# Optimization experiments

Hardware: AMD Instinct MI355X
Metric: run time of the kernel (lower is better)

The kernel has to match this reference:

```python
import jax, jax.numpy as jnp
import numpy as np

N_NODES = 100000
N_EDGES = 1600000
IN_DIM = 10
HID = 64
OUT_DIM = 2


def _gcn_norm(edge_index, num_nodes):
    # PyG gcn_norm with add_self_loops=False, edge_weight=1
    src, dst = edge_index[0], edge_index[1]
    deg = jnp.zeros((num_nodes,), jnp.float32).at[dst].add(1.0)
    dinv = jnp.where(deg > 0, jax.lax.rsqrt(deg), 0.0)
    return dinv[src] * dinv[dst]  # [E]


def _arma_conv(x, edge_index, norm, W, V, b):
    # ARMAConv, num_stacks=1, num_layers=1 (PyG defaults):
    # out = A_norm @ (x @ W_init) + x @ V_root + b   (no internal act at T=1)
    src, dst = edge_index[0], edge_index[1]
    h = x @ W                                   # [N, F_out]
    msg = norm[:, None] * h[src]                # [E, F_out] gather
    agg = jax.ops.segment_sum(msg, dst, num_segments=x.shape[0])  # scatter-add
    return agg + x @ V + b


def setup_inputs() -> dict:
    key = jax.random.key(0)
    ks = jax.random.split(key, 9)
    x = jax.random.uniform(ks[0], (N_NODES, IN_DIM), dtype=jnp.float32)
    edge_index = jax.random.randint(ks[1], (2, N_EDGES), 0, N_NODES, dtype=jnp.int64)
    s = 0.1
    W1 = jax.random.normal(ks[2], (IN_DIM, HID), jnp.float32) * s
    V1 = jax.random.normal(ks[3], (IN_DIM, HID), jnp.float32) * s
    b1 = jnp.zeros((HID,), jnp.float32)
    W2 = jax.random.normal(ks[4], (HID, HID), jnp.float32) * s
    V2 = jax.random.normal(ks[5], (HID, HID), jnp.float32) * s
    b2 = jnp.zeros((HID,), jnp.float32)
    W3 = jax.random.normal(ks[6], (HID, OUT_DIM), jnp.float32) * s
    V3 = jax.random.normal(ks[7], (HID, OUT_DIM), jnp.float32) * s
    b3 = jnp.zeros((OUT_DIM,), jnp.float32)
    return {"x": x, "edge_index": edge_index,
            "W1": W1, "V1": V1, "b1": b1,
            "W2": W2, "V2": V2, "b2": b2,
            "W3": W3, "V3": V3, "b3": b3}


def reference(x, edge_index, W1, V1, b1, W2, V2, b2, W3, V3, b3):
    norm = _gcn_norm(edge_index, x.shape[0])
    h = jax.nn.relu(_arma_conv(x, edge_index, norm, W1, V1, b1))
    # dropout is identity at eval time
    h = jax.nn.relu(_arma_conv(h, edge_index, norm, W2, V2, b2))
    h = _arma_conv(h, edge_index, norm, W3, V3, b3)
    return jax.nn.log_softmax(h, axis=1)
```

## Files before the change

### kernel.cpp

```cpp
#include <hip/hip_runtime.h>
#include <hip/hip_fp16.h>
#include <math.h>

#define NN 100000
#define NE 1600000
#define HID 64
#define BN 128
#define NBUCK 782
#define FBCAP 2304
#define NSB 49
#define SBCAP 34816
#define CHUNK1 4096
#define NBLK1 391
#define CSTRIDE 32

__device__ __forceinline__ __half2 shfl_xor_h2(__half2 v, int m) {
    unsigned int u = *(unsigned int*)&v;
    u = __shfl_xor(u, m);
    return *(__half2*)&u;
}
__device__ __forceinline__ unsigned int h2bits(__half2 v) {
    return *(unsigned int*)&v;
}


__global__ void k_zero_i(int* __restrict__ p, int n) {
    int i = blockIdx.x * blockDim.x + threadIdx.x;
    if (i < n) p[i] = 0;
}


__global__ __launch_bounds__(256) void k_binA1(const int* __restrict__ src,
                                               const int* __restrict__ dst,
                                               int* __restrict__ bcur1,
                                               unsigned int* __restrict__ sbdata) {
    __shared__ unsigned int par[CHUNK1];
    __shared__ unsigned short rnk[CHUNK1];
    __shared__ unsigned char bkt[CHUNK1];
    __shared__ int hist[NSB];
    __shared__ int base[NSB];
    int tid = threadIdx.x;
    int e0 = blockIdx.x * CHUNK1;
    int m = NE - e0; if (m > CHUNK1) m = CHUNK1;
    if (tid < NSB) hist[tid] = 0;
    __syncthreads();
    for (int i = tid; i < m; i += 256) {
        int s = src[e0 + i], d = dst[e0 + i];
        int b = d >> 11;
        par[i] = (unsigned int)s | ((unsigned int)(d & 2047) << 17);
        bkt[i] = (unsigned char)b;
        rnk[i] = (unsigned short)atomicAdd(&hist[b], 1);
    }
    __syncthreads();
    if (tid < NSB) {
        int h = hist[tid];
        base[tid] = h ? atomicAdd(&bcur1[tid * CSTRIDE], h) : 0;
    }
    __syncthreads();
    for (int i = tid; i < m; i += 256) {
        int b = bkt[i];
        int pos = base[b] + rnk[i];
        if (pos < SBCAP) sbdata[(size_t)b * SBCAP + pos] = par[i];
    }
}

__global__ __launch_bounds__(256) void k_binA2(const int* __restrict__ bcur1,
                                               const unsigned int* __restrict__ sbdata,
                                               int* __restrict__ bcur2,
                                               unsigned int* __restrict__ fbdata) {
    __shared__ unsigned int par[4352];
    __shared__ unsigned short rnk[4352];
    __shared__ unsigned char bkt[4352];
    __shared__ int hist[16];
    __shared__ int base[16];
    int tid = threadIdx.x;
    int sb = blockIdx.x >> 3, sl = blockIdx.x & 7;
    int m = bcur1[sb * CSTRIDE]; if (m > SBCAP) m = SBCAP;
    int L = (m + 7) >> 3;
    int lo = sl * L;
    int cnt = m - lo; if (cnt > L) cnt = L; if (cnt < 0) cnt = 0;
    if (tid < 16) hist[tid] = 0;
    __syncthreads();
    const unsigned int* sp = sbdata + (size_t)sb * SBCAP + lo;
    for (int i = tid; i < cnt; i += 256) {
        unsigned int u = sp[i];
        int dlow = (u >> 17) & 2047;
        int f = dlow >> 7;
        par[i] = (u & 0x1ffffu) | ((unsigned int)(dlow & 127) << 17);
        bkt[i] = (unsigned char)f;
        rnk[i] = (unsigned short)atomicAdd(&hist[f], 1);
    }
    __syncthreads();
    if (tid < 16) {
        int h = hist[tid];
        base[tid] = h ? atomicAdd(&bcur2[(sb * 16 + tid) * CSTRIDE], h) : 0;
    }
    __syncthreads();
    for (int i = tid; i < cnt; i += 256) {
        int f = bkt[i];
        int pos = base[f] + rnk[i];
        if (pos < FBCAP) fbdata[(size_t)(sb * 16 + f) * FBCAP + pos] = par[i];
    }
}

__global__ void k_bscan(const int* __restrict__ bcur2, int* __restrict__ ebase) {
    __shared__ int ls[16];
    int t = threadIdx.x;
    int lane = t & 63, wid = t >> 6;
    int v = 0;
    if (t < NBUCK) {
        int m = bcur2[t * CSTRIDE];
        v = (m < FBCAP) ? m : FBCAP;
    }
    int orig = v;
    for (int off = 1; off < 64; off <<= 1) {
        int u = __shfl_up(v, off);
        if (lane >= off) v += u;
    }
    if (lane == 63) ls[wid] = v;
    __syncthreads();
    if (wid == 0) {
        int w = (lane < 16) ? ls[lane] : 0;
        for (int off = 1; off < 16; off <<= 1) {
            int u = __shfl_up(w, off);
            if (lane >= off) w += u;
        }
        if (lane < 16) ls[lane] = w;
    }
    __syncthreads();
    int base = wid ? ls[wid - 1] : 0;
    int incl = base + v;
    if (t < NBUCK) ebase[t] = incl - orig;
    if (t == NBUCK - 1) ebase[NBUCK] = incl;
}

__global__ __launch_bounds__(128) void k_binB(const int* __restrict__ bcur2,
                                              const int* __restrict__ ebase,
                                              const unsigned int* __restrict__ fbdata,
                                              int* __restrict__ rp, float* __restrict__ dinv,
                                              int* __restrict__ perm) {
    __shared__ unsigned int se[FBCAP];
    __shared__ int cnt[BN];
    __shared__ int scn[BN];
    int b = blockIdx.x, tid = threadIdx.x;
    int m = bcur2[b * CSTRIDE]; if (m > FBCAP) m = FBCAP;
    int base = ebase[b];
    for (int i = tid; i < m; i += 128) se[i] = fbdata[(size_t)b * FBCAP + i];
    cnt[tid] = 0;
    __syncthreads();
    for (int i = tid; i < m; i += 128) atomicAdd(&cnt[se[i] >> 17], 1);
    __syncthreads();
    int c = cnt[tid];
    int g = b * BN + tid;
    if (g < NN) dinv[g] = (c > 0) ? rsqrtf((float)c) : 0.0f;
    scn[tid] = c;
    __syncthreads();
    for (int off = 1; off < 128; off <<= 1) {
        int u = (tid >= off) ? scn[tid - off] : 0;
        __syncthreads();
        scn[tid] += u;
        __syncthreads();
    }
    int excl = scn[tid] - c;
    if (g < NN) rp[g] = base + excl;
    if (b == NBUCK - 1 && tid == 0) rp[NN] = ebase[NBUCK];
    cnt[tid] = excl;
    __syncthreads();
    for (int i = tid; i < m; i += 128) {
        unsigned int u = se[i];
        int pos = atomicAdd(&cnt[u >> 17], 1);
        perm[base + pos] = (int)(u & 0x1ffffu);
    }
}


__global__ __launch_bounds__(256) void k_l1f(
        const int* __restrict__ rp, const int* __restrict__ perm,
        const float* __restrict__ dinv, const float* __restrict__ x,
        const float* __restrict__ W, const float* __restrict__ V,
        const float* __restrict__ b, unsigned short* __restrict__ th, int N) {
    __shared__ float sW[640], sV[640];
    for (int i = threadIdx.x; i < 640; i += 256) { sW[i] = W[i]; sV[i] = V[i]; }
    __syncthreads();
    int n = (blockIdx.x * 256 + threadIdx.x) >> 4;
    if (n >= N) return;
    int sub = threadIdx.x & 15;
    int beg = rp[n], end = rp[n + 1];
    float ag[10];
#pragma unroll
    for (int k = 0; k < 10; ++k) ag[k] = 0.0f;
    for (int j = beg + sub; j < end; j += 16) {
        int s = perm[j];
        float w = dinv[s];
        const float2* xr = (const float2*)(x + (size_t)s * 10);
        float2 v0 = xr[0], v1 = xr[1], v2 = xr[2], v3 = xr[3], v4 = xr[4];
        ag[0] += w * v0.x; ag[1] += w * v0.y; ag[2] += w * v1.x; ag[3] += w * v1.y;
        ag[4] += w * v2.x; ag[5] += w * v2.y; ag[6] += w * v3.x; ag[7] += w * v3.y;
        ag[8] += w * v4.x; ag[9] += w * v4.y;
    }
#pragma unroll
    for (int mk = 1; mk <= 8; mk <<= 1) {
#pragma unroll
        for (int k = 0; k < 10; ++k) ag[k] += __shfl_xor(ag[k], mk);
    }
    float dn = dinv[n];
#pragma unroll
    for (int k = 0; k < 10; ++k) ag[k] *= dn;
    const float2* xn = (const float2*)(x + (size_t)n * 10);
    float2 x0 = xn[0], x1 = xn[1], x2 = xn[2], x3 = xn[3], x4 = xn[4];
    float xv[10] = {x0.x, x0.y, x1.x, x1.y, x2.x, x2.y, x3.x, x3.y, x4.x, x4.y};
    int f0 = sub * 4;
    float4 bb = *(const float4*)(b + f0);
    float acc[4] = {bb.x, bb.y, bb.z, bb.w};
#pragma unroll
    for (int k = 0; k < 10; ++k) {
        float4 wq = *(const float4*)&sW[k * HID + f0];
        float4 vq = *(const float4*)&sV[k * HID + f0];
        acc[0] += ag[k] * wq.x + xv[k] * vq.x;
        acc[1] += ag[k] * wq.y + xv[k] * vq.y;
        acc[2] += ag[k] * wq.z + xv[k] * vq.z;
        acc[3] += ag[k] * wq.w + xv[k] * vq.w;
    }
    __half2 lo = __floats2half2_rn(fmaxf(acc[0], 0.0f), fmaxf(acc[1], 0.0f));
    __half2 hi = __floats2half2_rn(fmaxf(acc[2], 0.0f), fmaxf(acc[3], 0.0f));
    *(uint2*)(th + (size_t)n * HID + f0) = make_uint2(h2bits(lo), h2bits(hi));
}


__global__ __launch_bounds__(256) void k_agg64h(
        const int* __restrict__ rp, const int* __restrict__ perm,
        const float* __restrict__ dinv, const unsigned short* __restrict__ th,
        unsigned short* __restrict__ aggth, int N) {
    int wid = (blockIdx.x * blockDim.x + threadIdx.x) >> 6;
    if (wid >= N) return;
    int n = __builtin_amdgcn_readfirstlane(wid);
    int lane = threadIdx.x & 63;
    int grp = lane >> 3;
    int sub = lane & 7;
    int beg = rp[n], end = rp[n + 1];
    __half2 a0 = __float2half2_rn(0.0f), a1 = a0, a2 = a0, a3 = a0;
    for (int j = beg + grp; j < end; j += 8) {
        int s = perm[j];
        __half2 w2 = __float2half2_rn(dinv[s]);
        uint4 u = *(const uint4*)(th + (size_t)s * HID + sub * 8);
        a0 = __hfma2(w2, *(__half2*)&u.x, a0);
        a1 = __hfma2(w2, *(__half2*)&u.y, a1);
        a2 = __hfma2(w2, *(__half2*)&u.z, a2);
        a3 = __hfma2(w2, *(__half2*)&u.w, a3);
    }
#pragma unroll
    for (int m = 8; m < 64; m <<= 1) {
        a0 = __hadd2(a0, shfl_xor_h2(a0, m));
        a1 = __hadd2(a1, shfl_xor_h2(a1, m));
        a2 = __hadd2(a2, shfl_xor_h2(a2, m));
        a3 = __hadd2(a3, shfl_xor_h2(a3, m));
    }
    if (grp == 0) {
        __half2 dn2 = __float2half2_rn(dinv[n]);
        uint4 o;
        o.x = h2bits(__hmul2(dn2, a0));
        o.y = h2bits(__hmul2(dn2, a1));
        o.z = h2bits(__hmul2(dn2, a2));
        o.w = h2bits(__hmul2(dn2, a3));
        *(uint4*)(aggth + (size_t)n * HID + sub * 8) = o;
    }
}

__global__ __launch_bounds__(256) void k_agg3lsm(const int* __restrict__ rp,
                                                 const int* __restrict__ perm,
                                                 const float* __restrict__ dinv,
                                                 const float2* __restrict__ h3,
                                                 const float2* __restrict__ y3,
                                                 float* __restrict__ out, int N) {
    int n = (blockIdx.x * 256 + threadIdx.x) >> 4;
    if (n >= N) return;
    int sl = threadIdx.x & 15;
    int beg = rp[n], end = rp[n + 1];
    float a0 = 0.0f, a1 = 0.0f;
    for (int j = beg + sl; j < end; j += 16) {
        int s = perm[j];
        float w = dinv[s];
        float2 hh = h3[s];
        a0 += w * hh.x;
        a1 += w * hh.y;
    }
#pragma unroll
    for (int mk = 1; mk <= 8; mk <<= 1) {
        a0 += __shfl_xor(a0, mk);
        a1 += __shfl_xor(a1, mk);
    }
    if (sl == 0) {
        float dn = dinv[n];
        float2 yy = y3[n];
        float z0 = dn * a0 + yy.x;
        float z1 = dn * a1 + yy.y;
        float m = fmaxf(z0, z1);
        float l = m + logf(expf(z0 - m) + expf(z1 - m));
        out[n * 2 + 0] = z0 - l;
        out[n * 2 + 1] = z1 - l;
    }
}


__global__ __launch_bounds__(256) void k_dense23(
        const unsigned short* __restrict__ aggth, const unsigned short* __restrict__ th,
        const float* __restrict__ W, const float* __restrict__ V,
        const float* __restrict__ b, const float* __restrict__ W3,
        const float* __restrict__ V3, const float* __restrict__ b3,
        float2* __restrict__ h3, float2* __restrict__ y3, int N) {
    __shared__ __align__(16) float sA[64 * 64];
    __shared__ __align__(16) float sC[64 * 64];
    __shared__ __align__(16) float sW[64 * 64];
    __shared__ __align__(16) float sV[64 * 64];
    __shared__ float sW3[128], sV3[128];
    int tid = threadIdx.x;
    int base = blockIdx.x * 64;
    {
        const float4* W4 = (const float4*)W;
        const float4* V4 = (const float4*)V;
        float4* sW4 = (float4*)sW;
        float4* sV4 = (float4*)sV;
        for (int i = tid; i < 1024; i += 256) { sW4[i] = W4[i]; sV4[i] = V4[i]; }
        if (tid < 128) { sW3[tid] = W3[tid]; sV3[tid] = V3[tid]; }
    }
    {
        int n = tid >> 2;
        int ks = (tid & 3) * 16;
        int g = base + n;
        if (g < N) {
            const uint4* ar = (const uint4*)(aggth + (size_t)g * HID + ks);
            const uint4* cr = (const uint4*)(th + (size_t)g * HID + ks);
#pragma unroll
            for (int i = 0; i < 2; ++i) {
                uint4 ua = ar[i], uc = cr[i];
                int k = ks + 8 * i;
                float2 f;
                f = __half22float2(*(__half2*)&ua.x); sA[(k + 0) * 64 + n] = f.x; sA[(k + 1) * 64 + n] = f.y;
                f = __half22float2(*(__half2*)&ua.y); sA[(k + 2) * 64 + n] = f.x; sA[(k + 3) * 64 + n] = f.y;
                f = __half22float2(*(__half2*)&ua.z); sA[(k + 4) * 64 + n] = f.x; sA[(k + 5) * 64 + n] = f.y;
                f = __half22float2(*(__half2*)&ua.w); sA[(k + 6) * 64 + n] = f.x; sA[(k + 7) * 64 + n] = f.y;
                f = __half22float2(*(__half2*)&uc.x); sC[(k + 0) * 64 + n] = f.x; sC[(k + 1) * 64 + n] = f.y;
                f = __half22float2(*(__half2*)&uc.y); sC[(k + 2) * 64 + n] = f.x; sC[(k + 3) * 64 + n] = f.y;
                f = __half22float2(*(__half2*)&uc.z); sC[(k + 4) * 64 + n] = f.x; sC[(k + 5) * 64 + n] = f.y;
                f = __half22float2(*(__half2*)&uc.w); sC[(k + 6) * 64 + n] = f.x; sC[(k + 7) * 64 + n] = f.y;
            }
        } else {
#pragma unroll
            for (int i = 0; i < 16; ++i) {
                sA[(ks + i) * 64 + n] = 0.0f;
                sC[(ks + i) * 64 + n] = 0.0f;
            }
        }
    }
    __syncthreads();
    int tx = tid & 15, ty = tid >> 4;
    int f0 = tx * 4, n0 = ty * 4;
    float acc[4][4] = {};
#pragma unroll 8
    for (int k = 0; k < 64; ++k) {
        float4 a = *(const float4*)&sA[k * 64 + n0];
        float4 c = *(const float4*)&sC[k * 64 + n0];
        float4 w = *(const float4*)&sW[k * 64 + f0];
        float4 v = *(const float4*)&sV[k * 64 + f0];
        float aa[4] = {a.x, a.y, a.z, a.w}, cc[4] = {c.x, c.y, c.z, c.w};
        float ww[4] = {w.x, w.y, w.z, w.w}, vv[4] = {v.x, v.y, v.z, v.w};
#pragma unroll
        for (int i = 0; i < 4; ++i)
#pragma unroll
            for (int j = 0; j < 4; ++j)
                acc[i][j] += aa[i] * ww[j] + cc[i] * vv[j];
    }
    float4 bb = *(const float4*)&b[f0];
    float bv[4] = {bb.x, bb.y, bb.z, bb.w};
    float ph[4][2], py[4][2];
#pragma unroll
    for (int i = 0; i < 4; ++i) {
        float p0 = 0, p1 = 0, q0 = 0, q1 = 0;
#pragma unroll
        for (int j = 0; j < 4; ++j) {
            float tt = fmaxf(acc[i][j] + bv[j], 0.0f);
            int k = f0 + j;
            p0 += tt * sW3[k * 2 + 0];
            p1 += tt * sW3[k * 2 + 1];
            q0 += tt * sV3[k * 2 + 0];
            q1 += tt * sV3[k * 2 + 1];
        }
        ph[i][0] = p0; ph[i][1] = p1; py[i][0] = q0; py[i][1] = q1;
    }
#pragma unroll
    for (int mk = 1; mk <= 8; mk <<= 1) {
#pragma unroll
        for (int i = 0; i < 4; ++i) {
            ph[i][0] += __shfl_xor(ph[i][0], mk);
            ph[i][1] += __shfl_xor(ph[i][1], mk);
            py[i][0] += __shfl_xor(py[i][0], mk);
            py[i][1] += __shfl_xor(py[i][1], mk);
        }
    }
    if (tx == 0) {
        float b30 = b3[0], b31 = b3[1];
#pragma unroll
        for (int i = 0; i < 4; ++i) {
            int g = base + n0 + i;
            if (g < N) {
                h3[g] = make_float2(ph[i][0], ph[i][1]);
                y3[g] = make_float2(py[i][0] + b30, py[i][1] + b31);
            }
        }
    }
}


extern "C" void kernel_launch(void* const* d_in, const int* in_sizes, int n_in,
                              void* d_out, int out_size, void* d_ws, size_t ws_size,
                              hipStream_t stream) {
    const float* x  = (const float*)d_in[0];
    const int*   ei = (const int*)d_in[1];
    const int*   src = ei;
    const int*   dst = ei + NE;
    const float* W1 = (const float*)d_in[2];
    const float* V1 = (const float*)d_in[3];
    const float* b1 = (const float*)d_in[4];
    const float* W2 = (const float*)d_in[5];
    const float* V2 = (const float*)d_in[6];
    const float* b2 = (const float*)d_in[7];
    const float* W3 = (const float*)d_in[8];
    const float* V3 = (const float*)d_in[9];
    const float* b3 = (const float*)d_in[10];
    float* out = (float*)d_out;

    float* ws = (float*)d_ws;
    int*   bcur1 = (int*)ws;
    int*   bcur2 = (int*)(ws + 2048);
    int*   ebase = (int*)(ws + 27136);
    int*   rp    = (int*)(ws + 28160);
    float* dinv  = ws + 128512;
    unsigned int* sbdata = (unsigned int*)(ws + 228864);
    int*   perm  = (int*)(ws + 228864);
    unsigned int* fbdata = (unsigned int*)(ws + 1934848);
    float2* h3   = (float2*)(ws + 1934848);
    float2* y3   = (float2*)(ws + 1934848 + 2 * NN);
    unsigned short* aggth = (unsigned short*)(ws + 8334848);
    unsigned short* th    = (unsigned short*)(ws + 14734848);

    const int B = 256;

    k_zero_i<<<(27072 + B - 1) / B, B, 0, stream>>>(bcur1, 27072);
    k_binA1<<<NBLK1, B, 0, stream>>>(src, dst, bcur1, sbdata);
    k_binA2<<<NSB * 8, B, 0, stream>>>(bcur1, sbdata, bcur2, fbdata);
    k_bscan<<<1, 1024, 0, stream>>>(bcur2, ebase);
    k_binB<<<NBUCK, BN, 0, stream>>>(bcur2, ebase, fbdata, rp, dinv, perm);

    k_l1f<<<(NN * 16 + B - 1) / B, B, 0, stream>>>(rp, perm, dinv, x, W1, V1, b1, th, NN);

    k_agg64h<<<(NN * 64 + B - 1) / B, B, 0, stream>>>(rp, perm, dinv, th, aggth, NN);
    k_dense23<<<(NN + 63) / 64, B, 0, stream>>>(aggth, th, W2, V2, b2, W3, V3, b3,
                                                h3, y3, NN);

    k_agg3lsm<<<(NN * 16 + B - 1) / B, B, 0, stream>>>(rp, perm, dinv,
                                                       (const float2*)h3,
                                                       (const float2*)y3, out, NN);
}
```

Baseline: 246.2 us.

## Use fp16 MFMA for layer-2 dense transform in k_dense23

Replaces the fp32 FMA-based 64x128x64 GEMM in the fused layer-2/layer-3 dense kernel with 16x16x32 fp16 MFMA instructions. Activations stay in fp16 in shared memory with a padded row pitch, and the W/V weights are converted to fp16 and transposed into a single K=128 operand. The aim is to cut ALU time and shared-memory footprint, in exchange for rounding the weights to fp16. The output mapping is adapted to the MFMA accumulator layout.

After: 222.7 us. -9.6%, faster.

```diff
diff --git a/kernel.cpp b/kernel.cpp
--- a/kernel.cpp
+++ b/kernel.cpp
@@ -13,6 +13,10 @@
 #define CHUNK1 4096
 #define NBLK1 391
 #define CSTRIDE 32
+#define XPITCH 136
+
+typedef _Float16 half8 __attribute__((ext_vector_type(8)));
+typedef float floatx4 __attribute__((ext_vector_type(4)));
 
 __device__ __forceinline__ __half2 shfl_xor_h2(__half2 v, int m) {
     unsigned int u = *(unsigned int*)&v;
@@ -302,109 +306,96 @@
 }
 
 
-__global__ __launch_bounds__(256) void k_dense23(
+__global__ __launch_bounds__(256) void k_dense23m(
         const unsigned short* __restrict__ aggth, const unsigned short* __restrict__ th,
         const float* __restrict__ W, const float* __restrict__ V,
         const float* __restrict__ b, const float* __restrict__ W3,
         const float* __restrict__ V3, const float* __restrict__ b3,
         float2* __restrict__ h3, float2* __restrict__ y3, int N) {
-    __shared__ __align__(16) float sA[64 * 64];
-    __shared__ __align__(16) float sC[64 * 64];
-    __shared__ __align__(16) float sW[64 * 64];
-    __shared__ __align__(16) float sV[64 * 64];
+    __shared__ _Float16 sX[64 * XPITCH];
+    __shared__ _Float16 sWT[64 * XPITCH];
+    __shared__ float sB2[64];
     __shared__ float sW3[128], sV3[128];
     int tid = threadIdx.x;
     int base = blockIdx.x * 64;
     {
-        const float4* W4 = (const float4*)W;
-        const float4* V4 = (const float4*)V;
-        float4* sW4 = (float4*)sW;
-        float4* sV4 = (float4*)sV;
-        for (int i = tid; i < 1024; i += 256) { sW4[i] = W4[i]; sV4[i] = V4[i]; }
+        int f = tid & 63;
+        int g = tid >> 6;
+        const float* Wsrc = (g < 2) ? W : V;
+        int kbase = (g & 1) * 32;
+        int Kbase = (g < 2) ? kbase : (64 + kbase);
+#pragma unroll
+        for (int k2 = 0; k2 < 32; k2 += 2) {
+            float w0 = Wsrc[(kbase + k2) * 64 + f];
+            float w1 = Wsrc[(kbase + k2 + 1) * 64 + f];
+            __half2 h = __floats2half2_rn(w0, w1);
+            *(unsigned int*)&sWT[f * XPITCH + Kbase + k2] = h2bits(h);
+        }
+        if (tid < 64) sB2[tid] = b[tid];
         if (tid < 128) { sW3[tid] = W3[tid]; sV3[tid] = V3[tid]; }
     }
     {
-        int n = tid >> 2;
-        int ks = (tid & 3) * 16;
+        int n = tid >> 2, p = tid & 3;
         int g = base + n;
+        uint4 z = make_uint4(0, 0, 0, 0);
+        uint4 a0 = z, a1 = z, c0 = z, c1 = z;
         if (g < N) {
-            const uint4* ar = (const uint4*)(aggth + (size_t)g * HID + ks);
-            const uint4* cr = (const uint4*)(th + (size_t)g * HID + ks);
-#pragma unroll
-            for (int i = 0; i < 2; ++i) {
-                uint4 ua = ar[i], uc = cr[i];
-                int k = ks + 8 * i;
-                float2 f;
-                f = __half22float2(*(__half2*)&ua.x); sA[(k + 0) * 64 + n] = f.x; sA[(k + 1) * 64 + n] = f.y;
-                f = __half22float2(*(__half2*)&ua.y); sA[(k + 2) * 64 + n] = f.x; sA[(k + 3) * 64 + n] = f.y;
-                f = __half22float2(*(__half2*)&ua.z); sA[(k + 4) * 64 + n] = f.x; sA[(k + 5) * 64 + n] = f.y;
-                f = __half22float2(*(__half2*)&ua.w); sA[(k + 6) * 64 + n] = f.x; sA[(k + 7) * 64 + n] = f.y;
-                f = __half22float2(*(__half2*)&uc.x); sC[(k + 0) * 64 + n] = f.x; sC[(k + 1) * 64 + n] = f.y;
-                f = __half22float2(*(__half2*)&uc.y); sC[(k + 2) * 64 + n] = f.x; sC[(k + 3) * 64 + n] = f.y;
-                f = __half22float2(*(__half2*)&uc.z); sC[(k + 4) * 64 + n] = f.x; sC[(k + 5) * 64 + n] = f.y;
-                f = __half22float2(*(__half2*)&uc.w); sC[(k + 6) * 64 + n] = f.x; sC[(k + 7) * 64 + n] = f.y;
-            }
-        } else {
-#pragma unroll
-            for (int i = 0; i < 16; ++i) {
-                sA[(ks + i) * 64 + n] = 0.0f;
-                sC[(ks + i) * 64 + n] = 0.0f;
-            }
-        }
-    }
-    __syncthreads();
-    int tx = tid & 15, ty = tid >> 4;
-    int f0 = tx * 4, n0 = ty * 4;
-    float acc[4][4] = {};
-#pragma unroll 8
-    for (int k = 0; k < 64; ++k) {
-        float4 a = *(const float4*)&sA[k * 64 + n0];
-        float4 c = *(const float4*)&sC[k * 64 + n0];
-        float4 w = *(const float4*)&sW[k * 64 + f0];
-        float4 v = *(const float4*)&sV[k * 64 + f0];
-        float aa[4] = {a.x, a.y, a.z, a.w}, cc[4] = {c.x, c.y, c.z, c.w};
-        float ww[4] = {w.x, w.y, w.z, w.w}, vv[4] = {v.x, v.y, v.z, v.w};
-#pragma unroll
-        for (int i = 0; i < 4; ++i)
-#pragma unroll
-            for (int j = 0; j < 4; ++j)
-                acc[i][j] += aa[i] * ww[j] + cc[i] * vv[j];
-    }
-    float4 bb = *(const float4*)&b[f0];
-    float bv[4] = {bb.x, bb.y, bb.z, bb.w};
-    float ph[4][2], py[4][2];
-#pragma unroll
-    for (int i = 0; i < 4; ++i) {
-        float p0 = 0, p1 = 0, q0 = 0, q1 = 0;
-#pragma unroll
-        for (int j = 0; j < 4; ++j) {
-            float tt = fmaxf(acc[i][j] + bv[j], 0.0f);
-            int k = f0 + j;
-            p0 += tt * sW3[k * 2 + 0];
-            p1 += tt * sW3[k * 2 + 1];
-            q0 += tt * sV3[k * 2 + 0];
-            q1 += tt * sV3[k * 2 + 1];
-        }
-        ph[i][0] = p0; ph[i][1] = p1; py[i][0] = q0; py[i][1] = q1;
+            const uint4* ap = (const uint4*)(aggth + (size_t)g * HID + p * 16);
+            const uint4* cp = (const uint4*)(th + (size_t)g * HID + p * 16);
+            a0 = ap[0]; a1 = ap[1];
+            c0 = cp[0]; c1 = cp[1];
+        }
+        *(uint4*)&sX[n * XPITCH + p * 16] = a0;
+        *(uint4*)&sX[n * XPITCH + p * 16 + 8] = a1;
+        *(uint4*)&sX[n * XPITCH + 64 + p * 16] = c0;
+        *(uint4*)&sX[n * XPITCH + 64 + p * 16 + 8] = c1;
+    }
+    __syncthreads();
+    int lane = tid & 63;
+    int wv = tid >> 6;
+    int ml = lane & 15, quad = lane >> 4;
+    half8 a[4];
+#pragma unroll
+    for (int kt = 0; kt < 4; ++kt)
+        a[kt] = *(const half8*)&sX[(wv * 16 + ml) * XPITCH + kt * 32 + quad * 8];
+    float p0[4] = {}, p1[4] = {}, q0[4] = {}, q1[4] = {};
+#pragma unroll
+    for (int c = 0; c < 4; ++c) {
+        floatx4 acc = {0.0f, 0.0f, 0.0f, 0.0f};
+#pragma unroll
+        for (int kt = 0; kt < 4; ++kt) {
+            half8 bf = *(const half8*)&sWT[(c * 16 + ml) * XPITCH + kt * 32 + quad * 8];
+            acc = __builtin_amdgcn_mfma_f32_16x16x32_f16(a[kt], bf, acc, 0, 0, 0);
+        }
+        int col = c * 16 + ml;
+        float bias = sB2[col];
+        float w30 = sW3[col * 2], w31 = sW3[col * 2 + 1];
+        float v30 = sV3[col * 2], v31 = sV3[col * 2 + 1];
+#pragma unroll
+        for (int r = 0; r < 4; ++r) {
+            float t = fmaxf(acc[r] + bias, 0.0f);
+            p0[r] += t * w30; p1[r] += t * w31;
+            q0[r] += t * v30; q1[r] += t * v31;
+        }
     }
 #pragma unroll
     for (int mk = 1; mk <= 8; mk <<= 1) {
 #pragma unroll
-        for (int i = 0; i < 4; ++i) {
-            ph[i][0] += __shfl_xor(ph[i][0], mk);
-            ph[i][1] += __shfl_xor(ph[i][1], mk);
-            py[i][0] += __shfl_xor(py[i][0], mk);
-            py[i][1] += __shfl_xor(py[i][1], mk);
-        }
-    }
-    if (tx == 0) {
+        for (int r = 0; r < 4; ++r) {
+            p0[r] += __shfl_xor(p0[r], mk);
+            p1[r] += __shfl_xor(p1[r], mk);
+            q0[r] += __shfl_xor(q0[r], mk);
+            q1[r] += __shfl_xor(q1[r], mk);
+        }
+    }
+    if (ml == 0) {
         float b30 = b3[0], b31 = b3[1];
 #pragma unroll
-        for (int i = 0; i < 4; ++i) {
-            int g = base + n0 + i;
+        for (int r = 0; r < 4; ++r) {
+            int g = base + wv * 16 + quad * 4 + r;
             if (g < N) {
-                h3[g] = make_float2(ph[i][0], ph[i][1]);
-                y3[g] = make_float2(py[i][0] + b30, py[i][1] + b31);
+                h3[g] = make_float2(p0[r], p1[r]);
+                y3[g] = make_float2(q0[r] + b30, q1[r] + b31);
             }
         }
     }
@@ -454,8 +445,8 @@
     k_l1f<<<(NN * 16 + B - 1) / B, B, 0, stream>>>(rp, perm, dinv, x, W1, V1, b1, th, NN);
 
     k_agg64h<<<(NN * 64 + B - 1) / B, B, 0, stream>>>(rp, perm, dinv, th, aggth, NN);
-    k_dense23<<<(NN + 63) / 64, B, 0, stream>>>(aggth, th, W2, V2, b2, W3, V3, b3,
-                                                h3, y3, NN);
+    k_dense23m<<<(NN + 63) / 64, B, 0, stream>>>(aggth, th, W2, V2, b2, W3, V3, b3,
+                                                 h3, y3, NN);
 
     k_agg3lsm<<<(NN * 16 + B - 1) / B, B, 0, stream>>>(rp, perm, dinv,
                                                        (const float2*)h3,
```
